# Kernel optimization log

Measured on AMD Instinct MI355X. Metric: run time of the kernel, lower is better.

Reference implementation:

```python
import jax, jax.numpy as jnp
import numpy as np

N = 100000    # nodes
R = 8         # relations
HFR = 128     # input feature dim
HTO = 128     # output feature dim
NNZ = 1600000 # edges (nonzeros of the (N*R, N) sparse matrix)


def setup_inputs() -> dict:
    key = jax.random.key(0)
    k1, k2, k3, k4, k5 = jax.random.split(key, 5)
    nodes = jax.random.normal(k1, (N, HFR), dtype=jnp.float32)
    rows = jax.random.randint(k2, (NNZ,), 0, N * R)   # row index into (N*R, N) sparse matrix
    cols = jax.random.randint(k3, (NNZ,), 0, N)       # column = source node
    indices = jnp.stack([rows, cols]).astype(jnp.int64)
    values = jax.random.uniform(k4, (NNZ,), dtype=jnp.float32)
    # xavier-uniform-ish init for (r, hfr, hto) relation weights
    weights = jax.random.normal(k5, (R, HFR, HTO), dtype=jnp.float32) * np.float32(1.0 / np.sqrt(HFR))
    return {"nodes": nodes, "indices": indices, "values": values, "weights": weights}


def reference(nodes, indices, values, weights):
    # nodes: [n, hfr]; indices: [2, nnz]; values: [nnz]; weights: [r, hfr, hto]
    n = nodes.shape[0]
    r = weights.shape[0]
    rows, cols = indices[0], indices[1]
    # spmm: (n*r, n) sparse @ (n, hfr) dense -> (n*r, hfr)
    msgs = values[:, None] * nodes[cols]                      # [nnz, hfr] gather + scale
    agg = jax.ops.segment_sum(msgs, rows, num_segments=n * r)  # [n*r, hfr] scatter-add
    agg = agg.reshape(r, n, -1)                                # [r, n, hfr]
    # per-relation GEMM 'rij,rnj->nri' followed by sum over r, fused into one einsum
    out = jnp.einsum('rij,rnj->ni', weights, agg)              # [n, hto]
    return jax.nn.relu(out)
```

## Files before the change

kernel.cpp:

```cpp
#include <hip/hip_runtime.h>
#include <hip/hip_bf16.h>
#include <stdint.h>

#define HFR 128
#define HTO 128
#define LDN 136

typedef short short8 __attribute__((ext_vector_type(8)));
typedef float f32x4  __attribute__((ext_vector_type(4)));
typedef unsigned long long u64;

static __device__ __forceinline__ unsigned short f2bf(float x) {
    __hip_bfloat16 h = __float2bfloat16(x);
    return *reinterpret_cast<unsigned short*>(&h);
}
static __device__ __forceinline__ float bflo(unsigned int x) {
    return __uint_as_float(x << 16);
}
static __device__ __forceinline__ float bfhi(unsigned int x) {
    return __uint_as_float(x & 0xffff0000u);
}

__global__ __launch_bounds__(256) void zero_i32(int* __restrict__ p, int n) {
    int i = blockIdx.x * 256 + threadIdx.x;
    if (i < n) p[i] = 0;
}

__global__ __launch_bounds__(256)
void count_kernel(const int* __restrict__ rows, int* __restrict__ cnt,
                  int N, int nnz) {
    int e = blockIdx.x * 256 + threadIdx.x;
    if (e >= nnz) return;
    int row = rows[e];
    int r   = row / N;
    int dst = row - r * N;
    atomicAdd(&cnt[dst], 1);
}

__global__ __launch_bounds__(256)
void scan_reduce(const int* __restrict__ cnt, int* __restrict__ bsum, int N) {
    __shared__ int s[256];
    int t = threadIdx.x;
    int i = blockIdx.x * 256 + t;
    s[t] = (i < N) ? cnt[i] : 0;
    __syncthreads();
    for (int off = 128; off > 0; off >>= 1) {
        if (t < off) s[t] += s[t + off];
        __syncthreads();
    }
    if (t == 0) bsum[blockIdx.x] = s[0];
}

__global__ __launch_bounds__(1024)
void scan_block(int* __restrict__ bsum, int nb) {
    __shared__ int s[1024];
    int t = threadIdx.x;
    s[t] = (t < nb) ? bsum[t] : 0;
    __syncthreads();
    for (int off = 1; off < 1024; off <<= 1) {
        int o = (t >= off) ? s[t - off] : 0;
        __syncthreads();
        s[t] += o;
        __syncthreads();
    }
    if (t < nb) bsum[t] = (t == 0) ? 0 : s[t - 1];
}

__global__ __launch_bounds__(256)
void scan_final(int* __restrict__ cnt, const int* __restrict__ bsum, int N) {
    __shared__ int s[256];
    int t = threadIdx.x;
    int i = blockIdx.x * 256 + t;
    int v = (i < N) ? cnt[i] : 0;
    s[t] = v;
    __syncthreads();
    for (int off = 1; off < 256; off <<= 1) {
        int o = (t >= off) ? s[t - off] : 0;
        __syncthreads();
        s[t] += o;
        __syncthreads();
    }
    int ex = ((t == 0) ? 0 : s[t - 1]) + bsum[blockIdx.x];
    if (i < N) cnt[i] = ex;
}

__global__ __launch_bounds__(256)
void conv_weights(const float* __restrict__ weights, short8* __restrict__ Wf) {
    int id = blockIdx.x * 256 + threadIdx.x;
    int lane = id & 63;
    int kk   = (id >> 6) & 3;
    int j    = (id >> 8) & 7;
    int r    = id >> 11;
    int m = lane & 15, q = lane >> 4;
    const float* src = weights + (((size_t)r * HFR) + j * 16 + m) * HTO + kk * 32 + q * 8;
    short8 sv;
#pragma unroll
    for (int e = 0; e < 8; ++e) sv[e] = f2bf(src[e]);
    Wf[((r * 4 + kk) * 8 + j) * 64 + lane] = sv;
}

__global__ __launch_bounds__(256, 4)
void fused_tp(const float* __restrict__ nodes,
              const short8* __restrict__ Wf,
              __hip_bfloat16* __restrict__ H,
              const int* __restrict__ rows, const int* __restrict__ cols,
              const float* __restrict__ vals,
              int* __restrict__ cursor, u64* __restrict__ sorted,
              int N, int R, int nnz, int Tblocks) {
    __shared__ unsigned short nd[128 * LDN];

    if ((int)blockIdx.x >= Tblocks) {
        int e = (blockIdx.x - Tblocks) * 256 + threadIdx.x;
        if (e >= nnz) return;
        int row = rows[e];
        int r   = row / N;
        int dst = row - r * N;
        int pos = atomicAdd(&cursor[dst], 1);
        unsigned int lo = (unsigned int)cols[e] | ((unsigned int)r << 17);
        u64 rec = ((u64)__float_as_uint(vals[e]) << 32) | (u64)lo;
        sorted[pos] = rec;
        return;
    }

    const int t    = threadIdx.x;
    const int n0   = blockIdx.x * 128;
    const int lane = t & 63;
    const int w    = t >> 6;
    const int m    = lane & 15;
    const int quad = lane >> 4;
    const int q8   = quad * 8;
    const int w32  = w * 32;

    const float4* src4 = reinterpret_cast<const float4*>(nodes);
#pragma unroll
    for (int it = 0; it < 8; ++it) {
        int id  = t + 256 * it;
        int row = id >> 4;
        int k8  = id & 15;
        float4 v0 = make_float4(0.f, 0.f, 0.f, 0.f);
        float4 v1 = v0;
        if (n0 + row < N) {
            v0 = src4[(size_t)(n0 + row) * 32 + k8 * 2];
            v1 = src4[(size_t)(n0 + row) * 32 + k8 * 2 + 1];
        }
        short8 sv;
        sv[0] = f2bf(v0.x); sv[1] = f2bf(v0.y); sv[2] = f2bf(v0.z); sv[3] = f2bf(v0.w);
        sv[4] = f2bf(v1.x); sv[5] = f2bf(v1.y); sv[6] = f2bf(v1.z); sv[7] = f2bf(v1.w);
        *reinterpret_cast<short8*>(&nd[row * LDN + k8 * 8]) = sv;
    }
    __syncthreads();

    for (int r = 0; r < R; ++r) {
        const short8* wr = Wf + (size_t)r * 2048 + lane;

        f32x4 acc[2][8];
#pragma unroll
        for (int t2 = 0; t2 < 2; ++t2)
#pragma unroll
            for (int j = 0; j < 8; ++j) acc[t2][j] = (f32x4)(0.f);

#pragma unroll
        for (int kk = 0; kk < 4; ++kk) {
            short8 a0 = *reinterpret_cast<const short8*>(&nd[(w32 +      m) * LDN + kk * 32 + q8]);
            short8 a1 = *reinterpret_cast<const short8*>(&nd[(w32 + 16 + m) * LDN + kk * 32 + q8]);
#pragma unroll
            for (int j = 0; j < 8; ++j) {
                short8 b = wr[kk * 512 + j * 64];
                acc[0][j] = __builtin_amdgcn_mfma_f32_16x16x32_bf16(a0, b, acc[0][j], 0, 0, 0);
                acc[1][j] = __builtin_amdgcn_mfma_f32_16x16x32_bf16(a1, b, acc[1][j], 0, 0, 0);
            }
        }

#pragma unroll
        for (int t2 = 0; t2 < 2; ++t2) {
            int rowbase = n0 + w32 + t2 * 16 + quad * 4;
#pragma unroll
            for (int reg = 0; reg < 4; ++reg) {
                int n = rowbase + reg;
                if (n < N) {
                    __hip_bfloat16* dst = H + ((size_t)r * N + n) * HTO + m;
#pragma unroll
                    for (int j = 0; j < 8; ++j)
                        dst[j * 16] = __float2bfloat16(acc[t2][j][reg]);
                }
            }
        }
    }
}

__global__ __launch_bounds__(256)
void gather_kernel(const u64* __restrict__ sorted,
                   const int* __restrict__ cursor,
                   const __hip_bfloat16* __restrict__ H,
                   float* __restrict__ out, int N) {
    const int wave = threadIdx.x >> 6;
    const int lane = threadIdx.x & 63;
    const int n = blockIdx.x * 4 + wave;
    if (n >= N) return;

    int e         = (n == 0) ? 0 : cursor[n - 1];
    const int end = cursor[n];

    float a0 = 0.f, a1 = 0.f, b0 = 0.f, b1 = 0.f;
    float c0 = 0.f, c1 = 0.f, d0 = 0.f, d1 = 0.f;

    const unsigned short* Hu = reinterpret_cast<const unsigned short*>(H);

#define HROW(q) reinterpret_cast<const unsigned int*>( \
        Hu + ((((size_t)((unsigned int)(q) >> 17) & 7) * (size_t)N + \
               ((unsigned int)(q) & 0x1FFFF)) << 7))
#define VAL(q)  __uint_as_float((unsigned int)((q) >> 32))

    for (; e + 8 <= end; e += 8) {
        const u64* p = sorted + __builtin_amdgcn_readfirstlane(e);
        u64 q0 = p[0], q1 = p[1], q2 = p[2], q3 = p[3];
        u64 q4 = p[4], q5 = p[5], q6 = p[6], q7 = p[7];
        unsigned int x0 = HROW(q0)[lane];
        unsigned int x1 = HROW(q1)[lane];
        unsigned int x2 = HROW(q2)[lane];
        unsigned int x3 = HROW(q3)[lane];
        unsigned int x4 = HROW(q4)[lane];
        unsigned int x5 = HROW(q5)[lane];
        unsigned int x6 = HROW(q6)[lane];
        unsigned int x7 = HROW(q7)[lane];
        a0 = fmaf(bflo(x0), VAL(q0), a0); a1 = fmaf(bfhi(x0), VAL(q0), a1);
        b0 = fmaf(bflo(x1), VAL(q1), b0); b1 = fmaf(bfhi(x1), VAL(q1), b1);
        c0 = fmaf(bflo(x2), VAL(q2), c0); c1 = fmaf(bfhi(x2), VAL(q2), c1);
        d0 = fmaf(bflo(x3), VAL(q3), d0); d1 = fmaf(bfhi(x3), VAL(q3), d1);
        a0 = fmaf(bflo(x4), VAL(q4), a0); a1 = fmaf(bfhi(x4), VAL(q4), a1);
        b0 = fmaf(bflo(x5), VAL(q5), b0); b1 = fmaf(bfhi(x5), VAL(q5), b1);
        c0 = fmaf(bflo(x6), VAL(q6), c0); c1 = fmaf(bfhi(x6), VAL(q6), c1);
        d0 = fmaf(bflo(x7), VAL(q7), d0); d1 = fmaf(bfhi(x7), VAL(q7), d1);
    }
    for (; e + 2 <= end; e += 2) {
        const u64* p = sorted + __builtin_amdgcn_readfirstlane(e);
        u64 q0 = p[0], q1 = p[1];
        unsigned int x0 = HROW(q0)[lane];
        unsigned int x1 = HROW(q1)[lane];
        a0 = fmaf(bflo(x0), VAL(q0), a0); a1 = fmaf(bfhi(x0), VAL(q0), a1);
        b0 = fmaf(bflo(x1), VAL(q1), b0); b1 = fmaf(bfhi(x1), VAL(q1), b1);
    }
    if (e < end) {
        u64 q0 = sorted[e];
        unsigned int x0 = HROW(q0)[lane];
        a0 = fmaf(bflo(x0), VAL(q0), a0); a1 = fmaf(bfhi(x0), VAL(q0), a1);
    }
#undef HROW
#undef VAL

    float2 o;
    o.x = fmaxf(a0 + b0 + c0 + d0, 0.f);
    o.y = fmaxf(a1 + b1 + c1 + d1, 0.f);
    *reinterpret_cast<float2*>(out + (size_t)n * HTO + lane * 2) = o;
}

extern "C" void kernel_launch(void* const* d_in, const int* in_sizes, int n_in,
                              void* d_out, int out_size, void* d_ws, size_t ws_size,
                              hipStream_t stream) {
    const float* nodes   = (const float*)d_in[0];
    const int*   indices = (const int*)d_in[1];
    const float* vals    = (const float*)d_in[2];
    const float* weights = (const float*)d_in[3];

    const int N   = in_sizes[0] / HFR;
    const int nnz = in_sizes[1] / 2;
    const int R   = in_sizes[3] / (HFR * HTO);

    const int* rows = indices;
    const int* cols = indices + nnz;

    char* ws = (char*)d_ws;
    __hip_bfloat16* H = (__hip_bfloat16*)ws;
    size_t off = (size_t)R * N * HTO * sizeof(__hip_bfloat16);
    u64* sorted = (u64*)(ws + off);
    off += (size_t)nnz * sizeof(u64);
    int* cnt = (int*)(ws + off);
    off += (size_t)N * sizeof(int);
    int* bsum = (int*)(ws + off);
    off += 1024 * sizeof(int);

    const size_t WFBYTES = (size_t)R * 4 * 8 * 64 * sizeof(short8);
    short8* Wf;
    if (off + WFBYTES <= ws_size) {
        Wf = (short8*)(ws + off);
    } else {
        Wf = (short8*)((char*)d_out + (size_t)out_size - WFBYTES);
    }

    float* out = (float*)d_out;

    const int NB = (N + 255) / 256;
    const int Tblocks = (N + 127) / 128;
    const int Pblocks = (nnz + 255) / 256;

    conv_weights<<<(R * 4 * 8 * 64) / 256, 256, 0, stream>>>(weights, Wf);
    zero_i32<<<NB, 256, 0, stream>>>(cnt, N);
    count_kernel<<<Pblocks, 256, 0, stream>>>(rows, cnt, N, nnz);
    scan_reduce<<<NB, 256, 0, stream>>>(cnt, bsum, N);
    scan_block<<<1, 1024, 0, stream>>>(bsum, NB);
    scan_final<<<NB, 256, 0, stream>>>(cnt, bsum, N);
    fused_tp<<<Tblocks + Pblocks, 256, 0, stream>>>(nodes, Wf, H,
                                                    rows, cols, vals,
                                                    cnt, sorted, N, R, nnz, Tblocks);
    gather_kernel<<<(N + 3) / 4, 256, 0, stream>>>(sorted, cnt, H, out, N);
}
```

Measured before the change: 378.8 us.

## Aggregate-then-transform: sort by (relation,dst), accumulate tiles in LDS, then MFMA

Reorders the computation from transform-then-gather (precompute H = nodes·W_r for all relations, then gather bf16 rows per destination) to gather-then-transform. Edges are now bucketed by the full (relation, dst) row using a two-level scan over N*R counters. A single kernel per 64-node tile scatters scaled bf16 source rows into an fp32 LDS tile with shared atomics, then multiplies that tile by W_r with MFMA and accumulates across relations. This removes the large R*N*HTO intermediate write and read, but adds LDS atomics, more scan passes and barriers per relation, and an uneven edge split across waves.

Measured after the change: 1.501 ms. 296% more time.

```diff
diff --git a/kernel.cpp b/kernel.cpp
--- a/kernel.cpp
+++ b/kernel.cpp
@@ -4,89 +4,54 @@
 
 #define HFR 128
 #define HTO 128
-#define LDN 136
+#define LDF 132
+#define TILE 64
 
 typedef short short8 __attribute__((ext_vector_type(8)));
 typedef float f32x4  __attribute__((ext_vector_type(4)));
 typedef unsigned long long u64;
+typedef unsigned int uint;
 
 static __device__ __forceinline__ unsigned short f2bf(float x) {
     __hip_bfloat16 h = __float2bfloat16(x);
     return *reinterpret_cast<unsigned short*>(&h);
 }
-static __device__ __forceinline__ float bflo(unsigned int x) {
+static __device__ __forceinline__ float bflo(uint x) {
     return __uint_as_float(x << 16);
 }
-static __device__ __forceinline__ float bfhi(unsigned int x) {
+static __device__ __forceinline__ float bfhi(uint x) {
     return __uint_as_float(x & 0xffff0000u);
 }
 
-__global__ __launch_bounds__(256) void zero_i32(int* __restrict__ p, int n) {
-    int i = blockIdx.x * 256 + threadIdx.x;
-    if (i < n) p[i] = 0;
-}
-
-__global__ __launch_bounds__(256)
-void count_kernel(const int* __restrict__ rows, int* __restrict__ cnt,
-                  int N, int nnz) {
-    int e = blockIdx.x * 256 + threadIdx.x;
-    if (e >= nnz) return;
-    int row = rows[e];
-    int r   = row / N;
-    int dst = row - r * N;
-    atomicAdd(&cnt[dst], 1);
-}
-
-__global__ __launch_bounds__(256)
-void scan_reduce(const int* __restrict__ cnt, int* __restrict__ bsum, int N) {
-    __shared__ int s[256];
-    int t = threadIdx.x;
-    int i = blockIdx.x * 256 + t;
-    s[t] = (i < N) ? cnt[i] : 0;
-    __syncthreads();
-    for (int off = 128; off > 0; off >>= 1) {
-        if (t < off) s[t] += s[t + off];
-        __syncthreads();
-    }
-    if (t == 0) bsum[blockIdx.x] = s[0];
-}
-
-__global__ __launch_bounds__(1024)
-void scan_block(int* __restrict__ bsum, int nb) {
-    __shared__ int s[1024];
-    int t = threadIdx.x;
-    s[t] = (t < nb) ? bsum[t] : 0;
-    __syncthreads();
-    for (int off = 1; off < 1024; off <<= 1) {
-        int o = (t >= off) ? s[t - off] : 0;
-        __syncthreads();
-        s[t] += o;
-        __syncthreads();
-    }
-    if (t < nb) bsum[t] = (t == 0) ? 0 : s[t - 1];
-}
-
-__global__ __launch_bounds__(256)
-void scan_final(int* __restrict__ cnt, const int* __restrict__ bsum, int N) {
-    __shared__ int s[256];
-    int t = threadIdx.x;
-    int i = blockIdx.x * 256 + t;
-    int v = (i < N) ? cnt[i] : 0;
-    s[t] = v;
-    __syncthreads();
-    for (int off = 1; off < 256; off <<= 1) {
-        int o = (t >= off) ? s[t - off] : 0;
-        __syncthreads();
-        s[t] += o;
-        __syncthreads();
-    }
-    int ex = ((t == 0) ? 0 : s[t - 1]) + bsum[blockIdx.x];
-    if (i < N) cnt[i] = ex;
-}
-
-__global__ __launch_bounds__(256)
-void conv_weights(const float* __restrict__ weights, short8* __restrict__ Wf) {
-    int id = blockIdx.x * 256 + threadIdx.x;
+__global__ __launch_bounds__(256)
+void prep(const float* __restrict__ nodes, const float* __restrict__ weights,
+          unsigned short* __restrict__ ndbf, short8* __restrict__ Wf,
+          int* __restrict__ cnt, int NR, int N, int ZB, int CB) {
+    int b = blockIdx.x;
+    int t = threadIdx.x;
+    if (b < ZB) {
+        int i = b * 256 + t;
+        if (i < NR) cnt[i] = 0;
+        return;
+    }
+    b -= ZB;
+    if (b < CB) {
+        int id = b * 256 + t;
+        if (id < N * 16) {
+            int n  = id >> 4;
+            int k8 = id & 15;
+            const float4* s = reinterpret_cast<const float4*>(nodes);
+            float4 v0 = s[(size_t)n * 32 + k8 * 2];
+            float4 v1 = s[(size_t)n * 32 + k8 * 2 + 1];
+            short8 sv;
+            sv[0] = f2bf(v0.x); sv[1] = f2bf(v0.y); sv[2] = f2bf(v0.z); sv[3] = f2bf(v0.w);
+            sv[4] = f2bf(v1.x); sv[5] = f2bf(v1.y); sv[6] = f2bf(v1.z); sv[7] = f2bf(v1.w);
+            *reinterpret_cast<short8*>(&ndbf[(size_t)n * HFR + k8 * 8]) = sv;
+        }
+        return;
+    }
+    b -= CB;
+    int id = b * 256 + t;
     int lane = id & 63;
     int kk   = (id >> 6) & 3;
     int j    = (id >> 8) & 7;
@@ -99,159 +64,175 @@
     Wf[((r * 4 + kk) * 8 + j) * 64 + lane] = sv;
 }
 
+__global__ __launch_bounds__(256)
+void count_kernel(const int* __restrict__ rows, int* __restrict__ cnt, int nnz) {
+    int e = blockIdx.x * 256 + threadIdx.x;
+    if (e >= nnz) return;
+    atomicAdd(&cnt[rows[e]], 1);
+}
+
+__global__ __launch_bounds__(256)
+void scan_reduce(const int* __restrict__ cnt, int* __restrict__ bsum, int N) {
+    __shared__ int s[256];
+    int t = threadIdx.x;
+    int i = blockIdx.x * 256 + t;
+    s[t] = (i < N) ? cnt[i] : 0;
+    __syncthreads();
+    for (int off = 128; off > 0; off >>= 1) {
+        if (t < off) s[t] += s[t + off];
+        __syncthreads();
+    }
+    if (t == 0) bsum[blockIdx.x] = s[0];
+}
+
+__global__ __launch_bounds__(1024)
+void scan_block(int* __restrict__ bsum, int nb) {
+    __shared__ int s[1024];
+    int t = threadIdx.x;
+    s[t] = (t < nb) ? bsum[t] : 0;
+    __syncthreads();
+    for (int off = 1; off < 1024; off <<= 1) {
+        int o = (t >= off) ? s[t - off] : 0;
+        __syncthreads();
+        s[t] += o;
+        __syncthreads();
+    }
+    if (t < nb) bsum[t] = (t == 0) ? 0 : s[t - 1];
+}
+
+__global__ __launch_bounds__(256)
+void scan_final(int* __restrict__ cnt, const int* __restrict__ bsum, int N) {
+    __shared__ int s[256];
+    int t = threadIdx.x;
+    int i = blockIdx.x * 256 + t;
+    int v = (i < N) ? cnt[i] : 0;
+    s[t] = v;
+    __syncthreads();
+    for (int off = 1; off < 256; off <<= 1) {
+        int o = (t >= off) ? s[t - off] : 0;
+        __syncthreads();
+        s[t] += o;
+        __syncthreads();
+    }
+    int ex = ((t == 0) ? 0 : s[t - 1]) + bsum[blockIdx.x];
+    if (i < N) cnt[i] = ex;
+}
+
+__global__ __launch_bounds__(256)
+void place_kernel(const int* __restrict__ rows, const int* __restrict__ cols,
+                  const float* __restrict__ vals,
+                  int* __restrict__ cursor, u64* __restrict__ sorted,
+                  int N, int nnz) {
+    int e = blockIdx.x * 256 + threadIdx.x;
+    if (e >= nnz) return;
+    int row = rows[e];
+    int r   = row / N;
+    int dst = row - r * N;
+    int pos = atomicAdd(&cursor[row], 1);
+    uint lo = (uint)cols[e] | ((uint)(dst & (TILE - 1)) << 17);
+    sorted[pos] = ((u64)__float_as_uint(vals[e]) << 32) | (u64)lo;
+}
+
 __global__ __launch_bounds__(256, 4)
-void fused_tp(const float* __restrict__ nodes,
-              const short8* __restrict__ Wf,
-              __hip_bfloat16* __restrict__ H,
-              const int* __restrict__ rows, const int* __restrict__ cols,
-              const float* __restrict__ vals,
-              int* __restrict__ cursor, u64* __restrict__ sorted,
-              int N, int R, int nnz, int Tblocks) {
-    __shared__ unsigned short nd[128 * LDN];
-
-    if ((int)blockIdx.x >= Tblocks) {
-        int e = (blockIdx.x - Tblocks) * 256 + threadIdx.x;
-        if (e >= nnz) return;
-        int row = rows[e];
-        int r   = row / N;
-        int dst = row - r * N;
-        int pos = atomicAdd(&cursor[dst], 1);
-        unsigned int lo = (unsigned int)cols[e] | ((unsigned int)r << 17);
-        u64 rec = ((u64)__float_as_uint(vals[e]) << 32) | (u64)lo;
-        sorted[pos] = rec;
-        return;
-    }
+void mega(const unsigned short* __restrict__ ndbf,
+          const short8* __restrict__ Wf,
+          const u64* __restrict__ sorted,
+          const int* __restrict__ cursor,
+          float* __restrict__ out, int N, int R) {
+    __shared__ float tile[TILE * LDF];
 
     const int t    = threadIdx.x;
-    const int n0   = blockIdx.x * 128;
     const int lane = t & 63;
     const int w    = t >> 6;
     const int m    = lane & 15;
     const int quad = lane >> 4;
     const int q8   = quad * 8;
-    const int w32  = w * 32;
-
-    const float4* src4 = reinterpret_cast<const float4*>(nodes);
-#pragma unroll
-    for (int it = 0; it < 8; ++it) {
-        int id  = t + 256 * it;
-        int row = id >> 4;
-        int k8  = id & 15;
-        float4 v0 = make_float4(0.f, 0.f, 0.f, 0.f);
-        float4 v1 = v0;
-        if (n0 + row < N) {
-            v0 = src4[(size_t)(n0 + row) * 32 + k8 * 2];
-            v1 = src4[(size_t)(n0 + row) * 32 + k8 * 2 + 1];
-        }
-        short8 sv;
-        sv[0] = f2bf(v0.x); sv[1] = f2bf(v0.y); sv[2] = f2bf(v0.z); sv[3] = f2bf(v0.w);
-        sv[4] = f2bf(v1.x); sv[5] = f2bf(v1.y); sv[6] = f2bf(v1.z); sv[7] = f2bf(v1.w);
-        *reinterpret_cast<short8*>(&nd[row * LDN + k8 * 8]) = sv;
-    }
-    __syncthreads();
+    const int w16  = w * 16;
+    const int n0   = blockIdx.x * TILE;
+    const int nend = min(n0 + TILE, N);
+
+    const uint* nd32 = reinterpret_cast<const uint*>(ndbf);
+    float4* t4 = reinterpret_cast<float4*>(tile);
+
+    f32x4 acc[8];
+#pragma unroll
+    for (int j = 0; j < 8; ++j) acc[j] = (f32x4)(0.f);
+
+#define VAL(q)  __uint_as_float((uint)((q) >> 32))
+#define EDGE(q, x) {                                                         \
+        float v  = VAL(q);                                                   \
+        int   dl = (int)(((uint)(q) >> 17) & (TILE - 1));                    \
+        atomicAdd(&tile[dl * LDF + 2 * lane],     bflo(x) * v);              \
+        atomicAdd(&tile[dl * LDF + 2 * lane + 1], bfhi(x) * v);              \
+    }
+#define NDROW(q) nd32[((size_t)((uint)(q) & 0x1FFFF)) * 64 + lane]
 
     for (int r = 0; r < R; ++r) {
+#pragma unroll 4
+        for (int i = t; i < TILE * LDF / 4; i += 256)
+            t4[i] = make_float4(0.f, 0.f, 0.f, 0.f);
+        __syncthreads();
+
+        int rowid0 = r * N + n0;
+        int e0 = (rowid0 == 0) ? 0 : cursor[rowid0 - 1];
+        int e1 = cursor[r * N + nend - 1];
+        int cntE  = e1 - e0;
+        int chunk = (cntE + 3) >> 2;
+        int ce0 = e0 + w * chunk;
+        int ce1 = min(ce0 + chunk, e1);
+        int e = ce0;
+        for (; e + 8 <= ce1; e += 8) {
+            const u64* p = sorted + __builtin_amdgcn_readfirstlane(e);
+            u64 q0 = p[0], q1 = p[1], q2 = p[2], q3 = p[3];
+            u64 q4 = p[4], q5 = p[5], q6 = p[6], q7 = p[7];
+            uint x0 = NDROW(q0);
+            uint x1 = NDROW(q1);
+            uint x2 = NDROW(q2);
+            uint x3 = NDROW(q3);
+            uint x4 = NDROW(q4);
+            uint x5 = NDROW(q5);
+            uint x6 = NDROW(q6);
+            uint x7 = NDROW(q7);
+            EDGE(q0, x0) EDGE(q1, x1) EDGE(q2, x2) EDGE(q3, x3)
+            EDGE(q4, x4) EDGE(q5, x5) EDGE(q6, x6) EDGE(q7, x7)
+        }
+        for (; e < ce1; ++e) {
+            u64 q0 = sorted[e];
+            uint x0 = NDROW(q0);
+            EDGE(q0, x0)
+        }
+        __syncthreads();
+
         const short8* wr = Wf + (size_t)r * 2048 + lane;
-
-        f32x4 acc[2][8];
-#pragma unroll
-        for (int t2 = 0; t2 < 2; ++t2)
-#pragma unroll
-            for (int j = 0; j < 8; ++j) acc[t2][j] = (f32x4)(0.f);
-
 #pragma unroll
         for (int kk = 0; kk < 4; ++kk) {
-            short8 a0 = *reinterpret_cast<const short8*>(&nd[(w32 +      m) * LDN + kk * 32 + q8]);
-            short8 a1 = *reinterpret_cast<const short8*>(&nd[(w32 + 16 + m) * LDN + kk * 32 + q8]);
-#pragma unroll
-            for (int j = 0; j < 8; ++j) {
-                short8 b = wr[kk * 512 + j * 64];
-                acc[0][j] = __builtin_amdgcn_mfma_f32_16x16x32_bf16(a0, b, acc[0][j], 0, 0, 0);
-                acc[1][j] = __builtin_amdgcn_mfma_f32_16x16x32_bf16(a1, b, acc[1][j], 0, 0, 0);
-            }
-        }
-
-#pragma unroll
-        for (int t2 = 0; t2 < 2; ++t2) {
-            int rowbase = n0 + w32 + t2 * 16 + quad * 4;
-#pragma unroll
-            for (int reg = 0; reg < 4; ++reg) {
-                int n = rowbase + reg;
-                if (n < N) {
-                    __hip_bfloat16* dst = H + ((size_t)r * N + n) * HTO + m;
-#pragma unroll
-                    for (int j = 0; j < 8; ++j)
-                        dst[j * 16] = __float2bfloat16(acc[t2][j][reg]);
-                }
-            }
-        }
-    }
-}
-
-__global__ __launch_bounds__(256)
-void gather_kernel(const u64* __restrict__ sorted,
-                   const int* __restrict__ cursor,
-                   const __hip_bfloat16* __restrict__ H,
-                   float* __restrict__ out, int N) {
-    const int wave = threadIdx.x >> 6;
-    const int lane = threadIdx.x & 63;
-    const int n = blockIdx.x * 4 + wave;
-    if (n >= N) return;
-
-    int e         = (n == 0) ? 0 : cursor[n - 1];
-    const int end = cursor[n];
-
-    float a0 = 0.f, a1 = 0.f, b0 = 0.f, b1 = 0.f;
-    float c0 = 0.f, c1 = 0.f, d0 = 0.f, d1 = 0.f;
-
-    const unsigned short* Hu = reinterpret_cast<const unsigned short*>(H);
-
-#define HROW(q) reinterpret_cast<const unsigned int*>( \
-        Hu + ((((size_t)((unsigned int)(q) >> 17) & 7) * (size_t)N + \
-               ((unsigned int)(q) & 0x1FFFF)) << 7))
-#define VAL(q)  __uint_as_float((unsigned int)((q) >> 32))
-
-    for (; e + 8 <= end; e += 8) {
-        const u64* p = sorted + __builtin_amdgcn_readfirstlane(e);
-        u64 q0 = p[0], q1 = p[1], q2 = p[2], q3 = p[3];
-        u64 q4 = p[4], q5 = p[5], q6 = p[6], q7 = p[7];
-        unsigned int x0 = HROW(q0)[lane];
-        unsigned int x1 = HROW(q1)[lane];
-        unsigned int x2 = HROW(q2)[lane];
-        unsigned int x3 = HROW(q3)[lane];
-        unsigned int x4 = HROW(q4)[lane];
-        unsigned int x5 = HROW(q5)[lane];
-        unsigned int x6 = HROW(q6)[lane];
-        unsigned int x7 = HROW(q7)[lane];
-        a0 = fmaf(bflo(x0), VAL(q0), a0); a1 = fmaf(bfhi(x0), VAL(q0), a1);
-        b0 = fmaf(bflo(x1), VAL(q1), b0); b1 = fmaf(bfhi(x1), VAL(q1), b1);
-        c0 = fmaf(bflo(x2), VAL(q2), c0); c1 = fmaf(bfhi(x2), VAL(q2), c1);
-        d0 = fmaf(bflo(x3), VAL(q3), d0); d1 = fmaf(bfhi(x3), VAL(q3), d1);
-        a0 = fmaf(bflo(x4), VAL(q4), a0); a1 = fmaf(bfhi(x4), VAL(q4), a1);
-        b0 = fmaf(bflo(x5), VAL(q5), b0); b1 = fmaf(bfhi(x5), VAL(q5), b1);
-        c0 = fmaf(bflo(x6), VAL(q6), c0); c1 = fmaf(bfhi(x6), VAL(q6), c1);
-        d0 = fmaf(bflo(x7), VAL(q7), d0); d1 = fmaf(bfhi(x7), VAL(q7), d1);
-    }
-    for (; e + 2 <= end; e += 2) {
-        const u64* p = sorted + __builtin_amdgcn_readfirstlane(e);
-        u64 q0 = p[0], q1 = p[1];
-        unsigned int x0 = HROW(q0)[lane];
-        unsigned int x1 = HROW(q1)[lane];
-        a0 = fmaf(bflo(x0), VAL(q0), a0); a1 = fmaf(bfhi(x0), VAL(q0), a1);
-        b0 = fmaf(bflo(x1), VAL(q1), b0); b1 = fmaf(bfhi(x1), VAL(q1), b1);
-    }
-    if (e < end) {
-        u64 q0 = sorted[e];
-        unsigned int x0 = HROW(q0)[lane];
-        a0 = fmaf(bflo(x0), VAL(q0), a0); a1 = fmaf(bfhi(x0), VAL(q0), a1);
-    }
-#undef HROW
+            const float4* fp = reinterpret_cast<const float4*>(
+                &tile[(w16 + m) * LDF + kk * 32 + q8]);
+            float4 f0 = fp[0], f1 = fp[1];
+            short8 a;
+            a[0] = f2bf(f0.x); a[1] = f2bf(f0.y); a[2] = f2bf(f0.z); a[3] = f2bf(f0.w);
+            a[4] = f2bf(f1.x); a[5] = f2bf(f1.y); a[6] = f2bf(f1.z); a[7] = f2bf(f1.w);
+#pragma unroll
+            for (int j = 0; j < 8; ++j)
+                acc[j] = __builtin_amdgcn_mfma_f32_16x16x32_bf16(a, wr[kk * 512 + j * 64],
+                                                                 acc[j], 0, 0, 0);
+        }
+        __syncthreads();
+    }
+#undef NDROW
+#undef EDGE
 #undef VAL
 
-    float2 o;
-    o.x = fmaxf(a0 + b0 + c0 + d0, 0.f);
-    o.y = fmaxf(a1 + b1 + c1 + d1, 0.f);
-    *reinterpret_cast<float2*>(out + (size_t)n * HTO + lane * 2) = o;
+#pragma unroll
+    for (int reg = 0; reg < 4; ++reg) {
+        int n = n0 + w16 + quad * 4 + reg;
+        if (n < N) {
+            float* dst = out + (size_t)n * HTO + m;
+#pragma unroll
+            for (int j = 0; j < 8; ++j)
+                dst[j * 16] = fmaxf(acc[j][reg], 0.f);
+        }
+    }
 }
 
 extern "C" void kernel_launch(void* const* d_in, const int* in_sizes, int n_in,
@@ -265,42 +246,41 @@
     const int N   = in_sizes[0] / HFR;
     const int nnz = in_sizes[1] / 2;
     const int R   = in_sizes[3] / (HFR * HTO);
+    const int NR  = N * R;
 
     const int* rows = indices;
     const int* cols = indices + nnz;
 
     char* ws = (char*)d_ws;
-    __hip_bfloat16* H = (__hip_bfloat16*)ws;
-    size_t off = (size_t)R * N * HTO * sizeof(__hip_bfloat16);
+    unsigned short* ndbf = (unsigned short*)ws;
+    size_t off = (size_t)N * HFR * sizeof(unsigned short);
     u64* sorted = (u64*)(ws + off);
     off += (size_t)nnz * sizeof(u64);
     int* cnt = (int*)(ws + off);
-    off += (size_t)N * sizeof(int);
-    int* bsum = (int*)(ws + off);
+    off += (size_t)NR * sizeof(int);
+    const int NB1 = (NR + 255) / 256;
+    int* b1 = (int*)(ws + off);
+    off += (size_t)NB1 * sizeof(int);
+    int* b2 = (int*)(ws + off);
     off += 1024 * sizeof(int);
-
-    const size_t WFBYTES = (size_t)R * 4 * 8 * 64 * sizeof(short8);
-    short8* Wf;
-    if (off + WFBYTES <= ws_size) {
-        Wf = (short8*)(ws + off);
-    } else {
-        Wf = (short8*)((char*)d_out + (size_t)out_size - WFBYTES);
-    }
+    short8* Wf = (short8*)(ws + off);
 
     float* out = (float*)d_out;
 
-    const int NB = (N + 255) / 256;
-    const int Tblocks = (N + 127) / 128;
-    const int Pblocks = (nnz + 255) / 256;
-
-    conv_weights<<<(R * 4 * 8 * 64) / 256, 256, 0, stream>>>(weights, Wf);
-    zero_i32<<<NB, 256, 0, stream>>>(cnt, N);
-    count_kernel<<<Pblocks, 256, 0, stream>>>(rows, cnt, N, nnz);
-    scan_reduce<<<NB, 256, 0, stream>>>(cnt, bsum, N);
-    scan_block<<<1, 1024, 0, stream>>>(bsum, NB);
-    scan_final<<<NB, 256, 0, stream>>>(cnt, bsum, N);
-    fused_tp<<<Tblocks + Pblocks, 256, 0, stream>>>(nodes, Wf, H,
-                                                    rows, cols, vals,
-                                                    cnt, sorted, N, R, nnz, Tblocks);
-    gather_kernel<<<(N + 3) / 4, 256, 0, stream>>>(sorted, cnt, H, out, N);
-}
+    const int ZB  = NB1;
+    const int CB  = (N * 16 + 255) / 256;
+    const int WB  = (R * 4 * 8 * 64) / 256;
+    const int EB  = (nnz + 255) / 256;
+    const int NB2 = (NB1 + 255) / 256;
+    const int MB  = (N + TILE - 1) / TILE;
+
+    prep<<<ZB + CB + WB, 256, 0, stream>>>(nodes, weights, ndbf, Wf, cnt, NR, N, ZB, CB);
+    count_kernel<<<EB, 256, 0, stream>>>(rows, cnt, nnz);
+    scan_reduce<<<NB1, 256, 0, stream>>>(cnt, b1, NR);
+    scan_reduce<<<NB2, 256, 0, stream>>>(b1, b2, NB1);
+    scan_block<<<1, 1024, 0, stream>>>(b2, NB2);
+    scan_final<<<NB2, 256, 0, stream>>>(b1, b2, NB1);
+    scan_final<<<NB1, 256, 0, stream>>>(cnt, b1, NR);
+    place_kernel<<<EB, 256, 0, stream>>>(rows, cols, vals, cnt, sorted, N, nnz);
+    mega<<<MB, 256, 0, stream>>>(ndbf, Wf, sorted, cnt, out, N, R);
+}
```
